# Performance work log

Hardware: AMD Instinct MI355X
Metric: run time of the kernel (lower is better)

The kernel has to match this reference:

```python
import jax, jax.numpy as jnp
import numpy as np

THRESHOLD = 0.5
NEG_POS_RATIO = 3
ALPHA = 1.0
B, N_OBJ, N_PRIORS, N_CLASSES = 64, 32, 8732, 81


def xy_to_cxcy(xy):
    return jnp.concatenate([(xy[..., :2] + xy[..., 2:]) / 2.0, xy[..., 2:] - xy[..., :2]], axis=-1)


def cxcy_to_gcxgcy(cxcy, priors):
    return jnp.concatenate([
        (cxcy[..., :2] - priors[..., :2]) / (priors[..., 2:] / 10.0),
        jnp.log(cxcy[..., 2:] / priors[..., 2:]) * 5.0,
    ], axis=-1)


def jaccard(a, b):
    # a: [n,4], b: [m,4], both interpreted as (x1,y1,x2,y2) -- the original code
    # passes priors_cxcy directly (faithfully reproduced here).
    lt = jnp.maximum(a[:, None, :2], b[None, :, :2])
    rb = jnp.minimum(a[:, None, 2:], b[None, :, 2:])
    inter = jnp.prod(jnp.clip(rb - lt, 0.0, None), axis=-1)          # [n,m]
    area_a = jnp.prod(a[:, 2:] - a[:, :2], axis=-1)                  # [n]
    area_b = jnp.prod(b[:, 2:] - b[:, :2], axis=-1)                  # [m]
    return inter / (area_a[:, None] + area_b[None, :] - inter)


def _match(boxes_i, labels_i, priors_cxcy):
    # boxes_i: [n_obj,4] xy, labels_i: [n_obj] int, priors_cxcy: [n_priors,4]
    n_obj = boxes_i.shape[0]
    ov = jaccard(boxes_i, priors_cxcy)                               # [n_obj, n_priors]
    ov_for_prior = ov.max(axis=0)                                    # [n_priors]
    obj_for_prior = ov.argmax(axis=0)                                # [n_priors]
    prior_for_obj = ov.argmax(axis=1)                                # [n_obj]
    obj_for_prior = obj_for_prior.at[prior_for_obj].set(jnp.arange(n_obj))
    ov_for_prior = ov_for_prior.at[prior_for_obj].set(1.0)
    lab = labels_i[obj_for_prior]
    lab = jnp.where(ov_for_prior < THRESHOLD, 0, lab)                # background
    true_locs = cxcy_to_gcxgcy(xy_to_cxcy(boxes_i[obj_for_prior]), priors_cxcy)
    return true_locs, lab


def setup_inputs() -> dict:
    key = jax.random.key(0)
    k1, k2, k3, k4, k5, k6, k7 = jax.random.split(key, 7)
    predicted_locs = jax.random.normal(k1, (B, N_PRIORS, 4), dtype=jnp.float32)
    predicted_scores = jax.random.normal(k2, (B, N_PRIORS, N_CLASSES), dtype=jnp.float32)
    # valid gt boxes in xy form, inside [0,1]
    cxy = 0.15 + 0.7 * jax.random.uniform(k3, (B, N_OBJ, 2))
    wh = 0.05 + 0.25 * jax.random.uniform(k4, (B, N_OBJ, 2))
    boxes = jnp.clip(jnp.concatenate([cxy - wh / 2, cxy + wh / 2], axis=-1), 0.0, 1.0).astype(jnp.float32)
    labels = jax.random.randint(k5, (B, N_OBJ), 1, N_CLASSES)        # foreground classes
    # priors: cx,cy small, w,h large so that treating (cx,cy,w,h) as xy (as the
    # original code does in jaccard) still yields positive areas
    p_cxy = 0.4 * jax.random.uniform(k6, (N_PRIORS, 2))
    p_wh = 0.5 + 0.5 * jax.random.uniform(k7, (N_PRIORS, 2))
    priors_cxcy = jnp.concatenate([p_cxy, p_wh], axis=-1).astype(jnp.float32)
    return {
        "predicted_locs": predicted_locs,
        "predicted_scores": predicted_scores,
        "boxes": boxes,
        "labels": labels,
        "priors_cxcy": priors_cxcy,
    }


def multibox_loss(predicted_locs, predicted_scores, boxes, labels, priors_cxcy):
    n_priors = priors_cxcy.shape[0]
    true_locs, true_classes = jax.vmap(_match, in_axes=(0, 0, None))(boxes, labels, priors_cxcy)
    pos = true_classes != 0                                          # [B, n_priors]
    pos_f = pos.astype(predicted_locs.dtype)
    n_pos = pos.sum(axis=1)                                          # [B]
    n_pos_total = n_pos.sum().astype(jnp.float32)
    # nn.L1Loss(): mean over the 4 coords of positive priors
    loc_loss = (jnp.abs(predicted_locs - true_locs) * pos_f[..., None]).sum() / (n_pos_total * 4.0)
    # per-prior cross entropy
    logp = jax.nn.log_softmax(predicted_scores, axis=-1)             # [B,P,C]
    ce = -jnp.take_along_axis(logp, true_classes[..., None], axis=-1)[..., 0]  # [B,P]
    conf_pos = (ce * pos_f).sum()
    ce_neg = jnp.where(pos, 0.0, ce)
    ce_neg_sorted = -jnp.sort(-ce_neg, axis=1)                       # descending
    ranks = jnp.arange(n_priors)[None, :]
    hard = (ranks < (NEG_POS_RATIO * n_pos)[:, None]).astype(ce.dtype)
    conf_hard_neg = (ce_neg_sorted * hard).sum()
    conf_loss = (conf_hard_neg + conf_pos) / n_pos_total
    return conf_loss + ALPHA * loc_loss


def reference(predicted_locs, predicted_scores, boxes, labels, priors_cxcy):
    return multibox_loss(predicted_locs, predicted_scores, boxes, labels, priors_cxcy)
```

## Files before the change

### kernel.cpp

```cpp
#include <hip/hip_runtime.h>
#include <math.h>
#include <stdint.h>

#define BATCH 64
#define N_OBJ 32
#define NP 8732
#define NC 81
#define THRESH 0.5f
#define ROWS_PER_BLK 64


__device__ __forceinline__ float iou_box_prior(float x1, float y1, float x2, float y2,
                                               float areaA, float4 pr, float areaB) {
    float iw = fminf(x2, pr.z) - fmaxf(x1, pr.x); iw = fmaxf(iw, 0.f);
    float ih = fminf(y2, pr.w) - fmaxf(y1, pr.y); ih = fmaxf(ih, 0.f);
    float inter = iw * ih;
    return inter / (areaA + areaB - inter);
}

__global__ void k_match_prior(const float* __restrict__ boxes,
                              const float* __restrict__ priors,
                              float* __restrict__ ovp, int* __restrict__ objp,
                              int* __restrict__ n_pos, float* __restrict__ scal) {
    int i = blockIdx.y;
    int t = threadIdx.x;
    if (blockIdx.x == 0 && i == 0) {
        if (t < BATCH) n_pos[t] = 0;
        if (t < 3) scal[t] = 0.f;
    }
    __shared__ float bx[N_OBJ * 4];
    if (t < N_OBJ * 4) bx[t] = boxes[i * N_OBJ * 4 + t];
    __syncthreads();
    int p = blockIdx.x * blockDim.x + t;
    if (p >= NP) return;
    float4 pr = ((const float4*)priors)[p];
    float areaB = (pr.z - pr.x) * (pr.w - pr.y);
    float best = -1.0f; int bestj = 0;
    #pragma unroll
    for (int j = 0; j < N_OBJ; ++j) {
        float x1 = bx[j * 4 + 0], y1 = bx[j * 4 + 1], x2 = bx[j * 4 + 2], y2 = bx[j * 4 + 3];
        float areaA = (x2 - x1) * (y2 - y1);
        float v = iou_box_prior(x1, y1, x2, y2, areaA, pr, areaB);
        if (v > best) { best = v; bestj = j; }
    }
    ovp[i * NP + p] = best;
    objp[i * NP + p] = bestj;
}

__global__ void k_match_obj(const float* __restrict__ boxes,
                            const float* __restrict__ priors,
                            int* __restrict__ pfo) {
    int j = blockIdx.x, i = blockIdx.y;
    const float* bp = boxes + (i * N_OBJ + j) * 4;
    float x1 = bp[0], y1 = bp[1], x2 = bp[2], y2 = bp[3];
    float areaA = (x2 - x1) * (y2 - y1);
    float best = -1.f; int bestp = NP;
    for (int p = threadIdx.x; p < NP; p += blockDim.x) {
        float4 pr = ((const float4*)priors)[p];
        float areaB = (pr.z - pr.x) * (pr.w - pr.y);
        float v = iou_box_prior(x1, y1, x2, y2, areaA, pr, areaB);
        if (v > best) { best = v; bestp = p; }
    }
    __shared__ float sv[256];
    __shared__ int   si[256];
    int t = threadIdx.x;
    sv[t] = best; si[t] = bestp;
    __syncthreads();
    for (int s = 128; s > 0; s >>= 1) {
        if (t < s) {
            float v2 = sv[t + s]; int i2 = si[t + s];
            if (v2 > sv[t] || (v2 == sv[t] && i2 < si[t])) { sv[t] = v2; si[t] = i2; }
        }
        __syncthreads();
    }
    if (t == 0) pfo[i * N_OBJ + j] = si[0];
}

__global__ void k_force(const int* __restrict__ pfo,
                        float* __restrict__ ovp, int* __restrict__ objp) {
    int i = blockIdx.x * blockDim.x + threadIdx.x;
    if (i >= BATCH) return;
    for (int j = 0; j < N_OBJ; ++j) {
        int p = pfo[i * N_OBJ + j];
        objp[i * NP + p] = j;
        ovp[i * NP + p] = 1.0f;
    }
}

__global__ void __launch_bounds__(256)
k_ce(const float* __restrict__ scores,
     const float* __restrict__ plocs,
     const float* __restrict__ boxes,
     const int*   __restrict__ labels,
     const float* __restrict__ priors,
     const float* __restrict__ ovp,
     const int*   __restrict__ objp,
     float* __restrict__ ce_neg,
     int* __restrict__ n_pos, float* __restrict__ scal) {
    __shared__ __align__(16) float smem[ROWS_PER_BLK * NC];
    __shared__ float acc_cpos, acc_loc;
    __shared__ int   acc_np;
    int i  = blockIdx.y;
    int p0 = blockIdx.x * ROWS_PER_BLK;
    int rows = NP - p0; if (rows > ROWS_PER_BLK) rows = ROWS_PER_BLK;
    int t = threadIdx.x;
    if (t == 0) { acc_cpos = 0.f; acc_loc = 0.f; acc_np = 0; }

    const float4* g4 = (const float4*)(scores + ((size_t)i * NP + p0) * NC);
    float4* s4 = (float4*)smem;
    int cnt4 = (rows * NC) >> 2;
    for (int idx = t; idx < cnt4; idx += 256) s4[idx] = g4[idx];
    __syncthreads();

    int r = t >> 2, c = t & 3;
    bool active = (r < rows);
    const float* row = smem + r * NC;

    float m = -INFINITY;
    if (active) {
        for (int e = c; e < NC; e += 4) m = fmaxf(m, row[e]);
    }
    m = fmaxf(m, __shfl_xor(m, 1));
    m = fmaxf(m, __shfl_xor(m, 2));
    float s = 0.f;
    if (active) {
        for (int e = c; e < NC; e += 4) s += __expf(row[e] - m);
    }
    s += __shfl_xor(s, 1);
    s += __shfl_xor(s, 2);

    if (active && c == 0) {
        float lse = m + __logf(s);
        int gi = i * NP + p0 + r;
        int   obj = objp[gi];
        float ov  = ovp[gi];
        int   lab = (ov < THRESH) ? 0 : labels[i * N_OBJ + obj];
        float ce = lse - row[lab];
        if (lab != 0) {
            atomicAdd(&acc_np, 1);
            atomicAdd(&acc_cpos, ce);
            const float* bp = boxes + (i * N_OBJ + obj) * 4;
            float x1 = bp[0], y1 = bp[1], x2 = bp[2], y2 = bp[3];
            float bcx = (x1 + x2) * 0.5f, bcy = (y1 + y2) * 0.5f;
            float bw = x2 - x1, bh = y2 - y1;
            float4 pr = ((const float4*)priors)[p0 + r];
            float g0 = (bcx - pr.x) / (pr.z / 10.0f);
            float g1 = (bcy - pr.y) / (pr.w / 10.0f);
            float g2 = logf(bw / pr.z) * 5.0f;
            float g3 = logf(bh / pr.w) * 5.0f;
            const float* pl = plocs + (size_t)gi * 4;
            float l = fabsf(pl[0] - g0) + fabsf(pl[1] - g1)
                    + fabsf(pl[2] - g2) + fabsf(pl[3] - g3);
            atomicAdd(&acc_loc, l);
            ce_neg[gi] = 0.f;
        } else {
            ce_neg[gi] = ce;
        }
    }
    __syncthreads();
    if (t == 0 && acc_np > 0) {
        atomicAdd(&n_pos[i], acc_np);
        atomicAdd(&scal[0], acc_cpos);
        atomicAdd(&scal[2], acc_loc);
    }
}

__global__ void __launch_bounds__(256)
k_topk(const float* __restrict__ ce_neg,
       const int* __restrict__ n_pos, float* __restrict__ scal) {
    int i = blockIdx.x;
    int t = threadIdx.x;
    float x[35];
    #pragma unroll
    for (int j = 0; j < 35; ++j) {
        int p = t + j * 256;
        x[j] = (p < NP) ? ce_neg[i * NP + p] : 0.f;
    }
    int k = 3 * n_pos[i];
    if (k > NP) k = NP;
    if (k <= 0) return;

    __shared__ int   cnt_s[4];
    __shared__ float sum_s[4];
    unsigned lo = 0u, hi = 0x7F800001u;
    while (hi - lo > 1u) {
        unsigned mid = lo + ((hi - lo) >> 1);
        int c = 0;
        #pragma unroll
        for (int j = 0; j < 35; ++j) c += (__float_as_uint(x[j]) >= mid) ? 1 : 0;
        #pragma unroll
        for (int off = 32; off; off >>= 1) c += __shfl_xor(c, off);
        if ((t & 63) == 0) cnt_s[t >> 6] = c;
        __syncthreads();
        int total = cnt_s[0] + cnt_s[1] + cnt_s[2] + cnt_s[3];
        __syncthreads();
        if (total >= k) lo = mid; else hi = mid;
    }
    float vk = __uint_as_float(lo);

    float s = 0.f; int c = 0;
    #pragma unroll
    for (int j = 0; j < 35; ++j) {
        float v = x[j];
        if (v > vk) { s += v; c++; }
    }
    #pragma unroll
    for (int off = 32; off; off >>= 1) { s += __shfl_xor(s, off); c += __shfl_xor(c, off); }
    if ((t & 63) == 0) { sum_s[t >> 6] = s; cnt_s[t >> 6] = c; }
    __syncthreads();
    if (t == 0) {
        float st = sum_s[0] + sum_s[1] + sum_s[2] + sum_s[3];
        int   ct = cnt_s[0] + cnt_s[1] + cnt_s[2] + cnt_s[3];
        atomicAdd(&scal[1], st + (float)(k - ct) * vk);
    }
}

__global__ void k_final(const int* __restrict__ n_pos,
                        const float* __restrict__ scal, float* __restrict__ out) {
    if (threadIdx.x == 0) {
        int nt = 0;
        for (int i = 0; i < BATCH; ++i) nt += n_pos[i];
        float nf = (float)nt;
        out[0] = (scal[1] + scal[0]) / nf + scal[2] / (nf * 4.0f);
    }
}

extern "C" void kernel_launch(void* const* d_in, const int* in_sizes, int n_in,
                              void* d_out, int out_size, void* d_ws, size_t ws_size,
                              hipStream_t stream) {
    const float* plocs  = (const float*)d_in[0];
    const float* scores = (const float*)d_in[1];
    const float* boxes  = (const float*)d_in[2];
    const int*   labels = (const int*)d_in[3];
    const float* priors = (const float*)d_in[4];
    float* out = (float*)d_out;

    char* ws = (char*)d_ws;
    size_t bp = (size_t)BATCH * NP * 4;
    float* ovp    = (float*)(ws);
    int*   objp   = (int*)  (ws + bp);
    float* ce_neg = (float*)(ws + 2 * bp);
    int*   pfo    = (int*)  (ws + 3 * bp);
    int*   n_pos  = pfo + BATCH * N_OBJ;
    float* scal   = (float*)(n_pos + BATCH);

    hipLaunchKernelGGL(k_match_prior, dim3((NP + 255) / 256, BATCH), dim3(256), 0, stream,
                       boxes, priors, ovp, objp, n_pos, scal);
    hipLaunchKernelGGL(k_match_obj, dim3(N_OBJ, BATCH), dim3(256), 0, stream,
                       boxes, priors, pfo);
    hipLaunchKernelGGL(k_force, dim3(1), dim3(64), 0, stream, pfo, ovp, objp);
    hipLaunchKernelGGL(k_ce, dim3((NP + ROWS_PER_BLK - 1) / ROWS_PER_BLK, BATCH), dim3(256), 0, stream,
                       scores, plocs, boxes, labels, priors, ovp, objp, ce_neg, n_pos, scal);
    hipLaunchKernelGGL(k_topk, dim3(BATCH), dim3(256), 0, stream, ce_neg, n_pos, scal);
    hipLaunchKernelGGL(k_final, dim3(1), dim3(1), 0, stream, n_pos, scal, out);
}
```

Measured before the change: 191.7 us.

## Compute per-row softmax CE with 16-lane groups reading scores directly from global

The cross-entropy kernel no longer stages 64 score rows in shared memory. Each row now goes to a 16-lane group that loads its 81 logits straight into registers and reduces max and sum with shuffles, using 16 rows per block. This removes the shared-memory staging, the block barriers and the block-level accumulators, and gives more blocks in flight. In exchange, every positive prior now does its own global atomic on n_pos and the loss scalars, which can contend. The final kernel also sums n_pos with a wavefront shuffle instead of a serial loop.

```diff
diff --git a/kernel.cpp b/kernel.cpp
--- a/kernel.cpp
+++ b/kernel.cpp
@@ -7,7 +7,6 @@
 #define NP 8732
 #define NC 81
 #define THRESH 0.5f
-#define ROWS_PER_BLK 64
 
 
 __device__ __forceinline__ float iou_box_prior(float x1, float y1, float x2, float y2,
@@ -97,71 +96,63 @@
      const int*   __restrict__ objp,
      float* __restrict__ ce_neg,
      int* __restrict__ n_pos, float* __restrict__ scal) {
-    __shared__ __align__(16) float smem[ROWS_PER_BLK * NC];
-    __shared__ float acc_cpos, acc_loc;
-    __shared__ int   acc_np;
-    int i  = blockIdx.y;
-    int p0 = blockIdx.x * ROWS_PER_BLK;
-    int rows = NP - p0; if (rows > ROWS_PER_BLK) rows = ROWS_PER_BLK;
-    int t = threadIdx.x;
-    if (t == 0) { acc_cpos = 0.f; acc_loc = 0.f; acc_np = 0; }
-
-    const float4* g4 = (const float4*)(scores + ((size_t)i * NP + p0) * NC);
-    float4* s4 = (float4*)smem;
-    int cnt4 = (rows * NC) >> 2;
-    for (int idx = t; idx < cnt4; idx += 256) s4[idx] = g4[idx];
-    __syncthreads();
-
-    int r = t >> 2, c = t & 3;
-    bool active = (r < rows);
-    const float* row = smem + r * NC;
-
-    float m = -INFINITY;
-    if (active) {
-        for (int e = c; e < NC; e += 4) m = fmaxf(m, row[e]);
-    }
+    int i    = blockIdx.y;
+    int t    = threadIdx.x;
+    int wid  = t >> 6;
+    int lane = t & 63;
+    int sub  = lane >> 4;
+    int l    = lane & 15;
+    int p    = blockIdx.x * 16 + wid * 4 + sub;
+    if (p >= NP) return;
+
+    const float* row = scores + ((size_t)i * NP + p) * NC;
+    float x0 = row[l];
+    float x1 = row[l + 16];
+    float x2 = row[l + 32];
+    float x3 = row[l + 48];
+    float x4 = row[l + 64];
+    float x5 = (l == 0) ? row[80] : -INFINITY;
+
+    float m = fmaxf(fmaxf(fmaxf(x0, x1), fmaxf(x2, x3)), fmaxf(x4, x5));
     m = fmaxf(m, __shfl_xor(m, 1));
     m = fmaxf(m, __shfl_xor(m, 2));
-    float s = 0.f;
-    if (active) {
-        for (int e = c; e < NC; e += 4) s += __expf(row[e] - m);
-    }
+    m = fmaxf(m, __shfl_xor(m, 4));
+    m = fmaxf(m, __shfl_xor(m, 8));
+
+    float s = __expf(x0 - m) + __expf(x1 - m) + __expf(x2 - m)
+            + __expf(x3 - m) + __expf(x4 - m) + __expf(x5 - m);
     s += __shfl_xor(s, 1);
     s += __shfl_xor(s, 2);
-
-    if (active && c == 0) {
+    s += __shfl_xor(s, 4);
+    s += __shfl_xor(s, 8);
+
+    if (l == 0) {
         float lse = m + __logf(s);
-        int gi = i * NP + p0 + r;
+        int gi = i * NP + p;
         int   obj = objp[gi];
         float ov  = ovp[gi];
         int   lab = (ov < THRESH) ? 0 : labels[i * N_OBJ + obj];
         float ce = lse - row[lab];
         if (lab != 0) {
-            atomicAdd(&acc_np, 1);
-            atomicAdd(&acc_cpos, ce);
+            atomicAdd(&n_pos[i], 1);
+            atomicAdd(&scal[0], ce);
             const float* bp = boxes + (i * N_OBJ + obj) * 4;
-            float x1 = bp[0], y1 = bp[1], x2 = bp[2], y2 = bp[3];
-            float bcx = (x1 + x2) * 0.5f, bcy = (y1 + y2) * 0.5f;
-            float bw = x2 - x1, bh = y2 - y1;
-            float4 pr = ((const float4*)priors)[p0 + r];
+            float bx1 = bp[0], by1 = bp[1], bx2 = bp[2], by2 = bp[3];
+            float bcx = (bx1 + bx2) * 0.5f, bcy = (by1 + by2) * 0.5f;
+            float bw = bx2 - bx1, bh = by2 - by1;
+            float4 pr = ((const float4*)priors)[p];
             float g0 = (bcx - pr.x) / (pr.z / 10.0f);
             float g1 = (bcy - pr.y) / (pr.w / 10.0f);
             float g2 = logf(bw / pr.z) * 5.0f;
             float g3 = logf(bh / pr.w) * 5.0f;
             const float* pl = plocs + (size_t)gi * 4;
-            float l = fabsf(pl[0] - g0) + fabsf(pl[1] - g1)
-                    + fabsf(pl[2] - g2) + fabsf(pl[3] - g3);
-            atomicAdd(&acc_loc, l);
+            float ll = fabsf(pl[0] - g0) + fabsf(pl[1] - g1)
+                     + fabsf(pl[2] - g2) + fabsf(pl[3] - g3);
+            atomicAdd(&scal[2], ll);
             ce_neg[gi] = 0.f;
         } else {
             ce_neg[gi] = ce;
         }
-    }
-    __syncthreads();
-    if (t == 0 && acc_np > 0) {
-        atomicAdd(&n_pos[i], acc_np);
-        atomicAdd(&scal[0], acc_cpos);
-        atomicAdd(&scal[2], acc_loc);
     }
 }
 
@@ -217,10 +208,12 @@
 
 __global__ void k_final(const int* __restrict__ n_pos,
                         const float* __restrict__ scal, float* __restrict__ out) {
-    if (threadIdx.x == 0) {
-        int nt = 0;
-        for (int i = 0; i < BATCH; ++i) nt += n_pos[i];
-        float nf = (float)nt;
+    int t = threadIdx.x;
+    int v = (t < BATCH) ? n_pos[t] : 0;
+    #pragma unroll
+    for (int off = 32; off; off >>= 1) v += __shfl_xor(v, off);
+    if (t == 0) {
+        float nf = (float)v;
         out[0] = (scal[1] + scal[0]) / nf + scal[2] / (nf * 4.0f);
     }
 }
@@ -249,8 +242,8 @@
     hipLaunchKernelGGL(k_match_obj, dim3(N_OBJ, BATCH), dim3(256), 0, stream,
                        boxes, priors, pfo);
     hipLaunchKernelGGL(k_force, dim3(1), dim3(64), 0, stream, pfo, ovp, objp);
-    hipLaunchKernelGGL(k_ce, dim3((NP + ROWS_PER_BLK - 1) / ROWS_PER_BLK, BATCH), dim3(256), 0, stream,
+    hipLaunchKernelGGL(k_ce, dim3((NP + 15) / 16, BATCH), dim3(256), 0, stream,
                        scores, plocs, boxes, labels, priors, ovp, objp, ce_neg, n_pos, scal);
     hipLaunchKernelGGL(k_topk, dim3(BATCH), dim3(256), 0, stream, ce_neg, n_pos, scal);
-    hipLaunchKernelGGL(k_final, dim3(1), dim3(1), 0, stream, n_pos, scal, out);
-}
+    hipLaunchKernelGGL(k_final, dim3(1), dim3(64), 0, stream, n_pos, scal, out);
+}
```

New measurement: 251.8 us. 1.31x slower.
